# Kernel optimization log

Hardware: AMD Instinct MI355X
Metric: run time of the kernel (lower is better)

Reference implementation:

```python
import jax, jax.numpy as jnp
import numpy as np
from jax import lax

TOPK = 80
RADIUS_GAIN = 14.0
RADIUS_MIN = 1.5
RADIUS_MAX = 18.0


def _norm01(x, eps=1e-6):
    b = x.shape[0]
    flat = x.reshape(b, -1)
    mn = flat.min(axis=1).reshape(b, 1, 1, 1)
    mx = flat.max(axis=1).reshape(b, 1, 1, 1)
    return (x - mn) / (mx - mn + eps)


def _avg_pool9(x):
    # kernel 9, stride 1, pad 4, count_include_pad=True (torch default)
    s = lax.reduce_window(x, 0.0, lax.add, (1, 1, 9, 9), (1, 1, 1, 1),
                          [(0, 0), (0, 0), (4, 4), (4, 4)])
    return s / 81.0


def _max_pool5(x):
    return lax.reduce_window(x, -jnp.inf, lax.max, (1, 1, 5, 5), (1, 1, 1, 1),
                             [(0, 0), (0, 0), (2, 2), (2, 2)])


def setup_inputs() -> dict:
    key = jax.random.key(0)
    k1, k2 = jax.random.split(key)
    B, H, W = 8, 256, 256
    voxel_score_map = jax.random.uniform(k1, (B, 1, H, W), dtype=jnp.float32)
    depth = jax.random.uniform(k2, (B, 1, H, W), dtype=jnp.float32)
    return {"voxel_score_map": voxel_score_map, "depth": depth}


def reference(voxel_score_map, depth):
    dtype = voxel_score_map.dtype
    b, _, h, w = voxel_score_map.shape

    # _compact_connected_prior
    occ = (voxel_score_map > 0.2).astype(dtype)
    local_occ = _avg_pool9(occ)
    local_mass = _avg_pool9(voxel_score_map)
    compact = _norm01(local_occ * local_mass)
    score_map = voxel_score_map * compact

    # _gaussian_map: 5x5 max-pool NMS -> per-image top-k peaks
    pooled = _max_pool5(score_map)
    maxima = score_map * (score_map == pooled).astype(dtype)
    flat = maxima[:, 0].reshape(b, h * w)          # [b, h*w]
    vals, inds = lax.top_k(flat, TOPK)             # [b, k]
    vals = jnp.where(vals > 0, vals, jnp.zeros_like(vals))  # masked peaks splat 0
    ys = (inds // w).astype(dtype)
    xs = (inds % w).astype(dtype)

    z = jnp.take_along_axis(depth[:, 0].reshape(b, h * w), inds, axis=1)
    z = jnp.maximum(z, 0.001)
    radius = jnp.clip(RADIUS_GAIN / z, RADIUS_MIN, RADIUS_MAX)  # [b, k]
    sigma2 = (0.6 * radius) ** 2                                 # [b, k]

    yy = jnp.arange(h, dtype=dtype)
    xx = jnp.arange(w, dtype=dtype)
    dx = xx[None, None, None, :] - xs[:, :, None, None]   # [b, k, 1, w]
    dy = yy[None, None, :, None] - ys[:, :, None, None]   # [b, k, h, 1]
    d2 = dx ** 2 + dy ** 2                                 # [b, k, h, w]
    maps = vals[:, :, None, None] * jnp.exp(-d2 / (2.0 * sigma2[:, :, None, None] + 1e-6))
    gauss = maps.max(axis=1)[:, None]                      # [b, 1, h, w]
    return _norm01(gauss)
```

## Files before the change

### kernel.cpp

```cpp
#include <hip/hip_runtime.h>
#include <float.h>
#include <math.h>

#define BB 8
#define HH 256
#define WW 256
#define NPIX 65536
#define TOT (BB*NPIX)
#define KTOP 80
#define NTIL 64
#define TCAP 128
#define SELBINS 4096
#define SELCAP 2048
typedef unsigned long long ull;

__global__ void k_box9(const float* __restrict__ vsm, float* __restrict__ prod,
                       float* __restrict__ pmn, float* __restrict__ pmx) {
    int blk = blockIdx.x;
    int b = blk >> 6;
    int t = blk & 63;
    int ty0 = (t >> 3) << 5;
    int tx0 = (t & 7) << 5;
    int tid = threadIdx.x;

    __shared__ float val[40][40];
    __shared__ float rs_o[40][32];
    __shared__ float rs_m[40][32];

    for (int i = tid; i < 1600; i += 256) {
        int ly = i / 40, lx = i - ly * 40;
        int gy = ty0 - 4 + ly, gx = tx0 - 4 + lx;
        float v = 0.f;
        if (gy >= 0 && gy < HH && gx >= 0 && gx < WW)
            v = vsm[(b * HH + gy) * WW + gx];
        val[ly][lx] = v;
    }
    __syncthreads();

    for (int i = tid; i < 1280; i += 256) {
        int ly = i >> 5, lx = i & 31;
        float so = 0.f, sm = 0.f;
        #pragma unroll
        for (int d = 0; d < 9; ++d) {
            float v = val[ly][lx + d];
            so += (v > 0.2f) ? 1.f : 0.f;
            sm += v;
        }
        rs_o[ly][lx] = so;
        rs_m[ly][lx] = sm;
    }
    __syncthreads();

    int ox = tid & 31;
    int oy0 = (tid >> 5) << 2;
    float tmn = FLT_MAX, tmx = -FLT_MAX;
    #pragma unroll
    for (int j = 0; j < 4; ++j) {
        int oy = oy0 + j;
        float so = 0.f, sm = 0.f;
        #pragma unroll
        for (int d = 0; d < 9; ++d) {
            so += rs_o[oy + d][ox];
            sm += rs_m[oy + d][ox];
        }
        float p = (so * (1.f / 81.f)) * (sm * (1.f / 81.f));
        prod[(b * HH + ty0 + oy) * WW + tx0 + ox] = p;
        tmn = fminf(tmn, p);
        tmx = fmaxf(tmx, p);
    }

    __shared__ float smn[256], smx[256];
    smn[tid] = tmn; smx[tid] = tmx;
    __syncthreads();
    for (int off = 128; off > 0; off >>= 1) {
        if (tid < off) {
            smn[tid] = fminf(smn[tid], smn[tid + off]);
            smx[tid] = fmaxf(smx[tid], smx[tid + off]);
        }
        __syncthreads();
    }
    if (tid == 0) { pmn[blk] = smn[0]; pmx[blk] = smx[0]; }
}

__global__ void k_nms(const float* __restrict__ vsm, const float* __restrict__ prod,
                      const float* __restrict__ pmn, const float* __restrict__ pmx,
                      unsigned* __restrict__ bcnt, float* __restrict__ candV,
                      int* __restrict__ candI) {
    int blk = blockIdx.x;
    int b = blk >> 6;
    int t = blk & 63;
    int ty0 = (t >> 3) << 5;
    int tx0 = (t & 7) << 5;
    int tid = threadIdx.x;

    __shared__ float sred[2];
    if (tid < 64) {
        float mn = pmn[b * NTIL + tid];
        float mx = pmx[b * NTIL + tid];
        #pragma unroll
        for (int o = 32; o > 0; o >>= 1) {
            mn = fminf(mn, __shfl_xor(mn, o, 64));
            mx = fmaxf(mx, __shfl_xor(mx, o, 64));
        }
        if (tid == 0) { sred[0] = mn; sred[1] = mx; }
    }
    __syncthreads();
    float mnp = sred[0];
    float inv = 1.f / (sred[1] - mnp + 1e-6f);

    __shared__ float sc[36][36];
    __shared__ float hm[36][32];

    for (int i = tid; i < 1296; i += 256) {
        int ly = i / 36, lx = i - ly * 36;
        int gy = ty0 - 2 + ly, gx = tx0 - 2 + lx;
        float s = -FLT_MAX;
        if (gy >= 0 && gy < HH && gx >= 0 && gx < WW) {
            int idx = (b * HH + gy) * WW + gx;
            s = vsm[idx] * ((prod[idx] - mnp) * inv);
        }
        sc[ly][lx] = s;
    }
    __syncthreads();

    for (int i = tid; i < 1152; i += 256) {
        int ly = i >> 5, lx = i & 31;
        float m = sc[ly][lx];
        #pragma unroll
        for (int d = 1; d < 5; ++d) m = fmaxf(m, sc[ly][lx + d]);
        hm[ly][lx] = m;
    }
    __syncthreads();

    __shared__ unsigned scnt;
    __shared__ float bv[TCAP];
    __shared__ int bi[TCAP];
    if (tid == 0) scnt = 0;
    __syncthreads();

    int ox = tid & 31;
    int oy0 = (tid >> 5) << 2;
    #pragma unroll
    for (int j = 0; j < 4; ++j) {
        int oy = oy0 + j;
        float m = hm[oy][ox];
        #pragma unroll
        for (int d = 1; d < 5; ++d) m = fmaxf(m, hm[oy + d][ox]);
        float s = sc[oy + 2][ox + 2];
        if (s == m && s > 0.f) {
            unsigned p = atomicAdd(&scnt, 1u);
            if (p < TCAP) {
                bv[p] = s;
                bi[p] = (ty0 + oy) * WW + tx0 + ox;
            }
        }
    }
    __syncthreads();
    unsigned cnt = min(scnt, (unsigned)TCAP);
    if (tid == 0) bcnt[blk] = cnt;
    for (unsigned i = tid; i < cnt; i += 256) {
        candV[blk * TCAP + i] = bv[i];
        candI[blk * TCAP + i] = bi[i];
    }
}

__global__ void __launch_bounds__(1024)
k_topk(const float* __restrict__ depth, const unsigned* __restrict__ bcnt,
       const float* __restrict__ candV, const int* __restrict__ candI,
       float4* __restrict__ pk) {
    int b = blockIdx.x;
    int tid = threadIdx.x;
    __shared__ unsigned hist[SELBINS];
    __shared__ unsigned sc[1024];
    __shared__ ull keyAll[SELCAP];
    __shared__ unsigned bcs[NTIL];
    __shared__ int sBin;
    __shared__ unsigned sN;

    const float* cv = candV + b * NTIL * TCAP;
    const int* ci = candI + b * NTIL * TCAP;

    #pragma unroll
    for (int i = 0; i < SELBINS / 1024; ++i) hist[tid + i * 1024] = 0;
    if (tid < NTIL) bcs[tid] = bcnt[b * NTIL + tid];
    if (tid == 0) { sBin = 0; sN = 0; }
    __syncthreads();

    for (int i = tid; i < NTIL * TCAP; i += 1024) {
        int tile = i >> 7, o = i & (TCAP - 1);
        if ((unsigned)o < bcs[tile])
            atomicAdd(&hist[__float_as_uint(cv[i]) >> 19], 1u);
    }
    __syncthreads();

    int j0 = tid * 4;
    unsigned h0 = hist[j0], h1 = hist[j0 + 1], h2 = hist[j0 + 2], h3 = hist[j0 + 3];
    unsigned part = h0 + h1 + h2 + h3;
    sc[tid] = part;
    __syncthreads();
    for (int off = 1; off < 1024; off <<= 1) {
        unsigned v = (tid + off < 1024) ? sc[tid + off] : 0u;
        __syncthreads();
        sc[tid] += v;
        __syncthreads();
    }
    unsigned excl = sc[tid] - part;
    unsigned suf3 = excl + h3;
    unsigned suf2 = suf3 + h2;
    unsigned suf1 = suf2 + h1;
    unsigned suf0 = suf1 + h0;
    if (suf0 >= KTOP && suf0 - h0 < KTOP) sBin = j0;
    if (suf1 >= KTOP && suf1 - h1 < KTOP) sBin = j0 + 1;
    if (suf2 >= KTOP && suf2 - h2 < KTOP) sBin = j0 + 2;
    if (suf3 >= KTOP && suf3 - h3 < KTOP) sBin = j0 + 3;
    __syncthreads();

    int B = sBin;
    for (int i = tid; i < NTIL * TCAP; i += 1024) {
        int tile = i >> 7, o = i & (TCAP - 1);
        if ((unsigned)o < bcs[tile]) {
            unsigned bits = __float_as_uint(cv[i]);
            if ((int)(bits >> 19) >= B) {
                unsigned p = atomicAdd(&sN, 1u);
                if (p < SELCAP)
                    keyAll[p] = ((ull)bits << 32) | (ull)(0xFFFFFFFFu - (unsigned)ci[i]);
            }
        }
    }
    __syncthreads();
    unsigned n = min(sN, (unsigned)SELCAP);
    unsigned P = 128; while (P < n) P <<= 1;
    for (unsigned i = n + tid; i < P; i += 1024) keyAll[i] = 0ull;
    __syncthreads();

    for (unsigned k = 2; k <= P; k <<= 1) {
        for (unsigned j = k >> 1; j > 0; j >>= 1) {
            for (unsigned i = tid; i < P; i += 1024) {
                unsigned ixj = i ^ j;
                if (ixj > i) {
                    ull a = keyAll[i], c = keyAll[ixj];
                    bool up = ((i & k) == 0);
                    if (up ? (a > c) : (a < c)) { keyAll[i] = c; keyAll[ixj] = a; }
                }
            }
            __syncthreads();
        }
    }

    if (tid < KTOP) {
        unsigned K = min((unsigned)KTOP, n);
        float plog = -INFINITY, fx = 0.f, fy = 0.f, c = 0.f;
        if ((unsigned)tid < K) {
            ull key = keyAll[P - 1 - tid];
            unsigned bits = (unsigned)(key >> 32);
            int idx = (int)(0xFFFFFFFFu - (unsigned)(key & 0xFFFFFFFFu));
            float val = __uint_as_float(bits);
            plog = log2f(val);
            fx = (float)(idx & 255);
            fy = (float)(idx >> 8);
            float z = fmaxf(depth[b * NPIX + idx], 0.001f);
            float r = fminf(fmaxf(14.f / z, 1.5f), 18.f);
            float s2 = 0.36f * r * r;
            c = 1.44269504f / (2.f * s2 + 1e-6f);
        }
        pk[b * KTOP + tid] = make_float4(plog, fx, fy, c);
    }
}

__global__ void k_splat(const float4* __restrict__ pk, float* __restrict__ gauss,
                        float* __restrict__ gmn, float* __restrict__ gmx) {
    int blk = blockIdx.x;
    int b = blk >> 6;
    int y0 = (blk & 63) << 2;
    int x = threadIdx.x;

    __shared__ float4 lp[KTOP];
    if (x < KTOP) lp[x] = pk[b * KTOP + x];
    __syncthreads();

    float fx = (float)x;
    float fy = (float)y0;
    float g0 = -INFINITY, g1 = -INFINITY, g2 = -INFINITY, g3 = -INFINITY;
    #pragma unroll 4
    for (int k = 0; k < KTOP; ++k) {
        float4 q = lp[k];
        float dx = fx - q.y;
        float dx2 = dx * dx;
        float dy = fy - q.z;
        float d2;
        d2 = fmaf(dy, dy, dx2);           g0 = fmaxf(g0, fmaf(-d2, q.w, q.x));
        float dyb = dy + 1.f;
        d2 = fmaf(dyb, dyb, dx2);         g1 = fmaxf(g1, fmaf(-d2, q.w, q.x));
        float dyc = dy + 2.f;
        d2 = fmaf(dyc, dyc, dx2);         g2 = fmaxf(g2, fmaf(-d2, q.w, q.x));
        float dyd = dy + 3.f;
        d2 = fmaf(dyd, dyd, dx2);         g3 = fmaxf(g3, fmaf(-d2, q.w, q.x));
    }
    float v0 = exp2f(g0), v1 = exp2f(g1), v2 = exp2f(g2), v3 = exp2f(g3);
    int base = (b * HH + y0) * WW + x;
    gauss[base]          = v0;
    gauss[base + WW]     = v1;
    gauss[base + 2 * WW] = v2;
    gauss[base + 3 * WW] = v3;

    float tmn = fminf(fminf(v0, v1), fminf(v2, v3));
    float tmx = fmaxf(fmaxf(v0, v1), fmaxf(v2, v3));
    __shared__ float smn[256], smx[256];
    smn[x] = tmn; smx[x] = tmx;
    __syncthreads();
    for (int off = 128; off > 0; off >>= 1) {
        if (x < off) {
            smn[x] = fminf(smn[x], smn[x + off]);
            smx[x] = fmaxf(smx[x], smx[x + off]);
        }
        __syncthreads();
    }
    if (x == 0) { gmn[blk] = smn[0]; gmx[blk] = smx[0]; }
}

__global__ void k_norm(const float* __restrict__ gauss, const float* __restrict__ gmn,
                       const float* __restrict__ gmx, float* __restrict__ out) {
    int blk = blockIdx.x;
    int b = blk >> 6;
    int tid = threadIdx.x;

    __shared__ float sred[2];
    if (tid < 64) {
        float mn = gmn[b * NTIL + tid];
        float mx = gmx[b * NTIL + tid];
        #pragma unroll
        for (int o = 32; o > 0; o >>= 1) {
            mn = fminf(mn, __shfl_xor(mn, o, 64));
            mx = fmaxf(mx, __shfl_xor(mx, o, 64));
        }
        if (tid == 0) { sred[0] = mn; sred[1] = mx; }
    }
    __syncthreads();
    float mn = sred[0];
    float inv = 1.f / (sred[1] - mn + 1e-6f);

    int i = blk * 256 + tid;
    float4 v = ((const float4*)gauss)[i];
    v.x = (v.x - mn) * inv;
    v.y = (v.y - mn) * inv;
    v.z = (v.z - mn) * inv;
    v.w = (v.w - mn) * inv;
    ((float4*)out)[i] = v;
}

extern "C" void kernel_launch(void* const* d_in, const int* in_sizes, int n_in,
                              void* d_out, int out_size, void* d_ws, size_t ws_size,
                              hipStream_t stream) {
    const float* vsm   = (const float*)d_in[0];
    const float* depth = (const float*)d_in[1];
    float* out = (float*)d_out;

    float4* pk = (float4*)d_ws;
    float* prod = (float*)(pk + BB * KTOP);
    float* gauss = prod + TOT;
    float* pmn = gauss + TOT;
    float* pmx = pmn + BB * NTIL;
    float* gmn = pmx + BB * NTIL;
    float* gmx = gmn + BB * NTIL;
    unsigned* bcnt = (unsigned*)(gmx + BB * NTIL);
    float* candV = (float*)(bcnt + BB * NTIL);
    int* candI = (int*)(candV + BB * NTIL * TCAP);

    const int NBLK = BB * NTIL;

    k_box9 <<<NBLK, 256, 0, stream>>>(vsm, prod, pmn, pmx);
    k_nms  <<<NBLK, 256, 0, stream>>>(vsm, prod, pmn, pmx, bcnt, candV, candI);
    k_topk <<<BB, 1024, 0, stream>>>(depth, bcnt, candV, candI, pk);
    k_splat<<<NBLK, 256, 0, stream>>>(pk, gauss, gmn, gmx);
    k_norm <<<NBLK, 256, 0, stream>>>(gauss, gmn, gmx, out);
}
```

Measured before the change: 42.45 us.

## Fuse per-image top-k selection into splat kernel, recomputed per block

Removes the separate 8-block top-k kernel and the pk workspace round trip. Each splat block now redundantly computes its image's top-k via histogram, compaction and bitonic sort with 256 threads before splatting its rows. This aims to eliminate a launch and a low-parallelism serial stage, at the cost of 64x redundant selection work, extra L2 traffic and larger shared memory per block.

```diff
diff --git a/kernel.cpp b/kernel.cpp
--- a/kernel.cpp
+++ b/kernel.cpp
@@ -12,71 +12,51 @@
 #define TCAP 128
 #define SELBINS 4096
 #define SELCAP 2048
+#define NBLK (BB*NTIL)
 typedef unsigned long long ull;
 
 __global__ void k_box9(const float* __restrict__ vsm, float* __restrict__ prod,
                        float* __restrict__ pmn, float* __restrict__ pmx) {
     int blk = blockIdx.x;
-    int b = blk >> 6;
-    int t = blk & 63;
-    int ty0 = (t >> 3) << 5;
-    int tx0 = (t & 7) << 5;
+    int b = blk >> 6, t = blk & 63;
+    int ty0 = (t >> 3) << 5, tx0 = (t & 7) << 5;
     int tid = threadIdx.x;
-
     __shared__ float val[40][40];
     __shared__ float rs_o[40][32];
     __shared__ float rs_m[40][32];
-
     for (int i = tid; i < 1600; i += 256) {
         int ly = i / 40, lx = i - ly * 40;
         int gy = ty0 - 4 + ly, gx = tx0 - 4 + lx;
         float v = 0.f;
-        if (gy >= 0 && gy < HH && gx >= 0 && gx < WW)
-            v = vsm[(b * HH + gy) * WW + gx];
+        if (gy >= 0 && gy < HH && gx >= 0 && gx < WW) v = vsm[(b * HH + gy) * WW + gx];
         val[ly][lx] = v;
     }
     __syncthreads();
-
     for (int i = tid; i < 1280; i += 256) {
         int ly = i >> 5, lx = i & 31;
         float so = 0.f, sm = 0.f;
         #pragma unroll
-        for (int d = 0; d < 9; ++d) {
-            float v = val[ly][lx + d];
-            so += (v > 0.2f) ? 1.f : 0.f;
-            sm += v;
-        }
-        rs_o[ly][lx] = so;
-        rs_m[ly][lx] = sm;
-    }
-    __syncthreads();
-
-    int ox = tid & 31;
-    int oy0 = (tid >> 5) << 2;
+        for (int d = 0; d < 9; ++d) { float v = val[ly][lx + d]; so += (v > 0.2f) ? 1.f : 0.f; sm += v; }
+        rs_o[ly][lx] = so; rs_m[ly][lx] = sm;
+    }
+    __syncthreads();
+    int ox = tid & 31, oy0 = (tid >> 5) << 2;
     float tmn = FLT_MAX, tmx = -FLT_MAX;
     #pragma unroll
     for (int j = 0; j < 4; ++j) {
         int oy = oy0 + j;
         float so = 0.f, sm = 0.f;
         #pragma unroll
-        for (int d = 0; d < 9; ++d) {
-            so += rs_o[oy + d][ox];
-            sm += rs_m[oy + d][ox];
-        }
+        for (int d = 0; d < 9; ++d) { so += rs_o[oy + d][ox]; sm += rs_m[oy + d][ox]; }
         float p = (so * (1.f / 81.f)) * (sm * (1.f / 81.f));
         prod[(b * HH + ty0 + oy) * WW + tx0 + ox] = p;
-        tmn = fminf(tmn, p);
-        tmx = fmaxf(tmx, p);
-    }
-
+        tmn = fminf(tmn, p); tmx = fmaxf(tmx, p);
+    }
     __shared__ float smn[256], smx[256];
     smn[tid] = tmn; smx[tid] = tmx;
     __syncthreads();
     for (int off = 128; off > 0; off >>= 1) {
-        if (tid < off) {
-            smn[tid] = fminf(smn[tid], smn[tid + off]);
-            smx[tid] = fmaxf(smx[tid], smx[tid + off]);
-        }
+        if (tid < off) { smn[tid] = fminf(smn[tid], smn[tid + off]); smx[tid] = fmaxf(smx[tid], smx[tid + off]); }
         __syncthreads();
     }
     if (tid == 0) { pmn[blk] = smn[0]; pmx[blk] = smx[0]; }
@@ -87,30 +67,22 @@
                       unsigned* __restrict__ bcnt, float* __restrict__ candV,
                       int* __restrict__ candI) {
     int blk = blockIdx.x;
-    int b = blk >> 6;
-    int t = blk & 63;
-    int ty0 = (t >> 3) << 5;
-    int tx0 = (t & 7) << 5;
+    int b = blk >> 6, t = blk & 63;
+    int ty0 = (t >> 3) << 5, tx0 = (t & 7) << 5;
     int tid = threadIdx.x;
-
     __shared__ float sred[2];
     if (tid < 64) {
         float mn = pmn[b * NTIL + tid];
         float mx = pmx[b * NTIL + tid];
         #pragma unroll
-        for (int o = 32; o > 0; o >>= 1) {
-            mn = fminf(mn, __shfl_xor(mn, o, 64));
-            mx = fmaxf(mx, __shfl_xor(mx, o, 64));
-        }
+        for (int o = 32; o > 0; o >>= 1) { mn = fminf(mn, __shfl_xor(mn, o, 64)); mx = fmaxf(mx, __shfl_xor(mx, o, 64)); }
         if (tid == 0) { sred[0] = mn; sred[1] = mx; }
     }
     __syncthreads();
     float mnp = sred[0];
     float inv = 1.f / (sred[1] - mnp + 1e-6f);
-
     __shared__ float sc[36][36];
     __shared__ float hm[36][32];
-
     for (int i = tid; i < 1296; i += 256) {
         int ly = i / 36, lx = i - ly * 36;
         int gy = ty0 - 2 + ly, gx = tx0 - 2 + lx;
@@ -122,7 +94,6 @@
         sc[ly][lx] = s;
     }
     __syncthreads();
-
     for (int i = tid; i < 1152; i += 256) {
         int ly = i >> 5, lx = i & 31;
         float m = sc[ly][lx];
@@ -131,15 +102,12 @@
         hm[ly][lx] = m;
     }
     __syncthreads();
-
     __shared__ unsigned scnt;
     __shared__ float bv[TCAP];
     __shared__ int bi[TCAP];
     if (tid == 0) scnt = 0;
     __syncthreads();
-
-    int ox = tid & 31;
-    int oy0 = (tid >> 5) << 2;
+    int ox = tid & 31, oy0 = (tid >> 5) << 2;
     #pragma unroll
     for (int j = 0; j < 4; ++j) {
         int oy = oy0 + j;
@@ -149,10 +117,7 @@
         float s = sc[oy + 2][ox + 2];
         if (s == m && s > 0.f) {
             unsigned p = atomicAdd(&scnt, 1u);
-            if (p < TCAP) {
-                bv[p] = s;
-                bi[p] = (ty0 + oy) * WW + tx0 + ox;
-            }
+            if (p < TCAP) { bv[p] = s; bi[p] = (ty0 + oy) * WW + tx0 + ox; }
         }
     }
     __syncthreads();
@@ -164,158 +129,153 @@
     }
 }
 
-__global__ void __launch_bounds__(1024)
-k_topk(const float* __restrict__ depth, const unsigned* __restrict__ bcnt,
-       const float* __restrict__ candV, const int* __restrict__ candI,
-       float4* __restrict__ pk) {
-    int b = blockIdx.x;
+__global__ void __launch_bounds__(256)
+k_splatk(const float* __restrict__ depth, const unsigned* __restrict__ bcnt,
+         const float* __restrict__ candV, const int* __restrict__ candI,
+         float* __restrict__ gauss, float* __restrict__ gmn, float* __restrict__ gmx) {
+    int blk = blockIdx.x;
+    int b = blk >> 6;
     int tid = threadIdx.x;
-    __shared__ unsigned hist[SELBINS];
-    __shared__ unsigned sc[1024];
-    __shared__ ull keyAll[SELCAP];
-    __shared__ unsigned bcs[NTIL];
+
+    __shared__ struct {
+        unsigned hist[SELBINS];
+        ull keyAll[SELCAP];
+        unsigned bcs[NTIL];
+        unsigned scan[256];
+    } tk;
+    __shared__ float4 lp[KTOP];
+    __shared__ float r0[256], r1[256];
     __shared__ int sBin;
     __shared__ unsigned sN;
 
-    const float* cv = candV + b * NTIL * TCAP;
-    const int* ci = candI + b * NTIL * TCAP;
-
-    #pragma unroll
-    for (int i = 0; i < SELBINS / 1024; ++i) hist[tid + i * 1024] = 0;
-    if (tid < NTIL) bcs[tid] = bcnt[b * NTIL + tid];
-    if (tid == 0) { sBin = 0; sN = 0; }
-    __syncthreads();
-
-    for (int i = tid; i < NTIL * TCAP; i += 1024) {
-        int tile = i >> 7, o = i & (TCAP - 1);
-        if ((unsigned)o < bcs[tile])
-            atomicAdd(&hist[__float_as_uint(cv[i]) >> 19], 1u);
-    }
-    __syncthreads();
-
-    int j0 = tid * 4;
-    unsigned h0 = hist[j0], h1 = hist[j0 + 1], h2 = hist[j0 + 2], h3 = hist[j0 + 3];
-    unsigned part = h0 + h1 + h2 + h3;
-    sc[tid] = part;
-    __syncthreads();
-    for (int off = 1; off < 1024; off <<= 1) {
-        unsigned v = (tid + off < 1024) ? sc[tid + off] : 0u;
-        __syncthreads();
-        sc[tid] += v;
-        __syncthreads();
-    }
-    unsigned excl = sc[tid] - part;
-    unsigned suf3 = excl + h3;
-    unsigned suf2 = suf3 + h2;
-    unsigned suf1 = suf2 + h1;
-    unsigned suf0 = suf1 + h0;
-    if (suf0 >= KTOP && suf0 - h0 < KTOP) sBin = j0;
-    if (suf1 >= KTOP && suf1 - h1 < KTOP) sBin = j0 + 1;
-    if (suf2 >= KTOP && suf2 - h2 < KTOP) sBin = j0 + 2;
-    if (suf3 >= KTOP && suf3 - h3 < KTOP) sBin = j0 + 3;
-    __syncthreads();
-
-    int B = sBin;
-    for (int i = tid; i < NTIL * TCAP; i += 1024) {
-        int tile = i >> 7, o = i & (TCAP - 1);
-        if ((unsigned)o < bcs[tile]) {
-            unsigned bits = __float_as_uint(cv[i]);
-            if ((int)(bits >> 19) >= B) {
-                unsigned p = atomicAdd(&sN, 1u);
-                if (p < SELCAP)
-                    keyAll[p] = ((ull)bits << 32) | (ull)(0xFFFFFFFFu - (unsigned)ci[i]);
-            }
-        }
-    }
-    __syncthreads();
-    unsigned n = min(sN, (unsigned)SELCAP);
-    unsigned P = 128; while (P < n) P <<= 1;
-    for (unsigned i = n + tid; i < P; i += 1024) keyAll[i] = 0ull;
-    __syncthreads();
-
-    for (unsigned k = 2; k <= P; k <<= 1) {
-        for (unsigned j = k >> 1; j > 0; j >>= 1) {
-            for (unsigned i = tid; i < P; i += 1024) {
-                unsigned ixj = i ^ j;
-                if (ixj > i) {
-                    ull a = keyAll[i], c = keyAll[ixj];
-                    bool up = ((i & k) == 0);
-                    if (up ? (a > c) : (a < c)) { keyAll[i] = c; keyAll[ixj] = a; }
+    {
+        const float* cv = candV + b * NTIL * TCAP;
+        const int*   ci = candI + b * NTIL * TCAP;
+        for (int i = tid; i < SELBINS; i += 256) tk.hist[i] = 0;
+        if (tid < NTIL) tk.bcs[tid] = bcnt[b * NTIL + tid];
+        if (tid == 0) { sBin = 0; sN = 0; }
+        __syncthreads();
+
+        for (int i = tid; i < NTIL * TCAP; i += 256) {
+            int tile = i >> 7, o = i & (TCAP - 1);
+            if ((unsigned)o < tk.bcs[tile])
+                atomicAdd(&tk.hist[__float_as_uint(cv[i]) >> 19], 1u);
+        }
+        __syncthreads();
+
+        int j0 = tid * 16;
+        unsigned part = 0;
+        #pragma unroll
+        for (int j = 0; j < 16; ++j) part += tk.hist[j0 + j];
+        tk.scan[tid] = part;
+        __syncthreads();
+        for (int off = 1; off < 256; off <<= 1) {
+            unsigned v = (tid + off < 256) ? tk.scan[tid + off] : 0u;
+            __syncthreads();
+            tk.scan[tid] += v;
+            __syncthreads();
+        }
+        unsigned run = tk.scan[tid] - part;
+        for (int j = 15; j >= 0; --j) {
+            unsigned h = tk.hist[j0 + j];
+            run += h;
+            if (run >= KTOP && run - h < KTOP) sBin = j0 + j;
+        }
+        __syncthreads();
+
+        int B = sBin;
+        for (int i = tid; i < NTIL * TCAP; i += 256) {
+            int tile = i >> 7, o = i & (TCAP - 1);
+            if ((unsigned)o < tk.bcs[tile]) {
+                unsigned bits = __float_as_uint(cv[i]);
+                if ((int)(bits >> 19) >= B) {
+                    unsigned p = atomicAdd(&sN, 1u);
+                    if (p < SELCAP)
+                        tk.keyAll[p] = ((ull)bits << 32) | (ull)(0xFFFFFFFFu - (unsigned)ci[i]);
                 }
             }
+        }
+        __syncthreads();
+        unsigned n = min(sN, (unsigned)SELCAP);
+        unsigned P = 128; while (P < n) P <<= 1;
+        for (unsigned i = n + tid; i < P; i += 256) tk.keyAll[i] = 0ull;
+        __syncthreads();
+
+        for (unsigned k = 2; k <= P; k <<= 1) {
+            for (unsigned j = k >> 1; j > 0; j >>= 1) {
+                for (unsigned i = tid; i < P; i += 256) {
+                    unsigned ixj = i ^ j;
+                    if (ixj > i) {
+                        ull a = tk.keyAll[i], c = tk.keyAll[ixj];
+                        bool up = ((i & k) == 0);
+                        if (up ? (a > c) : (a < c)) { tk.keyAll[i] = c; tk.keyAll[ixj] = a; }
+                    }
+                }
+                __syncthreads();
+            }
+        }
+
+        if (tid < KTOP) {
+            unsigned K = min((unsigned)KTOP, n);
+            float plog = -INFINITY, fx = 0.f, fy = 0.f, c = 0.f;
+            if ((unsigned)tid < K) {
+                ull key = tk.keyAll[P - 1 - tid];
+                unsigned bits = (unsigned)(key >> 32);
+                int idx = (int)(0xFFFFFFFFu - (unsigned)(key & 0xFFFFFFFFu));
+                float val = __uint_as_float(bits);
+                plog = log2f(val);
+                fx = (float)(idx & 255);
+                fy = (float)(idx >> 8);
+                float z = fmaxf(depth[b * NPIX + idx], 0.001f);
+                float r = fminf(fmaxf(14.f / z, 1.5f), 18.f);
+                float s2 = 0.36f * r * r;
+                c = 1.44269504f / (2.f * s2 + 1e-6f);
+            }
+            lp[tid] = make_float4(plog, fx, fy, c);
+        }
+        __syncthreads();
+    }
+
+    {
+        int y0 = (blk & 63) << 2;
+        float fx = (float)tid;
+        float fy = (float)y0;
+        float g0 = -INFINITY, g1 = -INFINITY, g2 = -INFINITY, g3 = -INFINITY;
+        #pragma unroll 4
+        for (int k = 0; k < KTOP; ++k) {
+            float4 q = lp[k];
+            float dx = fx - q.y;
+            float dx2 = dx * dx;
+            float dy = fy - q.z;
+            float d2;
+            d2 = fmaf(dy, dy, dx2);          g0 = fmaxf(g0, fmaf(-d2, q.w, q.x));
+            float dyb = dy + 1.f;
+            d2 = fmaf(dyb, dyb, dx2);        g1 = fmaxf(g1, fmaf(-d2, q.w, q.x));
+            float dyc = dy + 2.f;
+            d2 = fmaf(dyc, dyc, dx2);        g2 = fmaxf(g2, fmaf(-d2, q.w, q.x));
+            float dyd = dy + 3.f;
+            d2 = fmaf(dyd, dyd, dx2);        g3 = fmaxf(g3, fmaf(-d2, q.w, q.x));
+        }
+        float v0 = exp2f(g0), v1 = exp2f(g1), v2 = exp2f(g2), v3 = exp2f(g3);
+        int base = (b * HH + y0) * WW + tid;
+        gauss[base]          = v0;
+        gauss[base + WW]     = v1;
+        gauss[base + 2 * WW] = v2;
+        gauss[base + 3 * WW] = v3;
+
+        float tmn = fminf(fminf(v0, v1), fminf(v2, v3));
+        float tmx = fmaxf(fmaxf(v0, v1), fmaxf(v2, v3));
+        r0[tid] = tmn; r1[tid] = tmx;
+        __syncthreads();
+        for (int off = 128; off > 0; off >>= 1) {
+            if (tid < off) {
+                r0[tid] = fminf(r0[tid], r0[tid + off]);
+                r1[tid] = fmaxf(r1[tid], r1[tid + off]);
+            }
             __syncthreads();
         }
-    }
-
-    if (tid < KTOP) {
-        unsigned K = min((unsigned)KTOP, n);
-        float plog = -INFINITY, fx = 0.f, fy = 0.f, c = 0.f;
-        if ((unsigned)tid < K) {
-            ull key = keyAll[P - 1 - tid];
-            unsigned bits = (unsigned)(key >> 32);
-            int idx = (int)(0xFFFFFFFFu - (unsigned)(key & 0xFFFFFFFFu));
-            float val = __uint_as_float(bits);
-            plog = log2f(val);
-            fx = (float)(idx & 255);
-            fy = (float)(idx >> 8);
-            float z = fmaxf(depth[b * NPIX + idx], 0.001f);
-            float r = fminf(fmaxf(14.f / z, 1.5f), 18.f);
-            float s2 = 0.36f * r * r;
-            c = 1.44269504f / (2.f * s2 + 1e-6f);
-        }
-        pk[b * KTOP + tid] = make_float4(plog, fx, fy, c);
-    }
-}
-
-__global__ void k_splat(const float4* __restrict__ pk, float* __restrict__ gauss,
-                        float* __restrict__ gmn, float* __restrict__ gmx) {
-    int blk = blockIdx.x;
-    int b = blk >> 6;
-    int y0 = (blk & 63) << 2;
-    int x = threadIdx.x;
-
-    __shared__ float4 lp[KTOP];
-    if (x < KTOP) lp[x] = pk[b * KTOP + x];
-    __syncthreads();
-
-    float fx = (float)x;
-    float fy = (float)y0;
-    float g0 = -INFINITY, g1 = -INFINITY, g2 = -INFINITY, g3 = -INFINITY;
-    #pragma unroll 4
-    for (int k = 0; k < KTOP; ++k) {
-        float4 q = lp[k];
-        float dx = fx - q.y;
-        float dx2 = dx * dx;
-        float dy = fy - q.z;
-        float d2;
-        d2 = fmaf(dy, dy, dx2);           g0 = fmaxf(g0, fmaf(-d2, q.w, q.x));
-        float dyb = dy + 1.f;
-        d2 = fmaf(dyb, dyb, dx2);         g1 = fmaxf(g1, fmaf(-d2, q.w, q.x));
-        float dyc = dy + 2.f;
-        d2 = fmaf(dyc, dyc, dx2);         g2 = fmaxf(g2, fmaf(-d2, q.w, q.x));
-        float dyd = dy + 3.f;
-        d2 = fmaf(dyd, dyd, dx2);         g3 = fmaxf(g3, fmaf(-d2, q.w, q.x));
-    }
-    float v0 = exp2f(g0), v1 = exp2f(g1), v2 = exp2f(g2), v3 = exp2f(g3);
-    int base = (b * HH + y0) * WW + x;
-    gauss[base]          = v0;
-    gauss[base + WW]     = v1;
-    gauss[base + 2 * WW] = v2;
-    gauss[base + 3 * WW] = v3;
-
-    float tmn = fminf(fminf(v0, v1), fminf(v2, v3));
-    float tmx = fmaxf(fmaxf(v0, v1), fmaxf(v2, v3));
-    __shared__ float smn[256], smx[256];
-    smn[x] = tmn; smx[x] = tmx;
-    __syncthreads();
-    for (int off = 128; off > 0; off >>= 1) {
-        if (x < off) {
-            smn[x] = fminf(smn[x], smn[x + off]);
-            smx[x] = fmaxf(smx[x], smx[x + off]);
-        }
-        __syncthreads();
-    }
-    if (x == 0) { gmn[blk] = smn[0]; gmx[blk] = smx[0]; }
+        if (tid == 0) { gmn[blk] = r0[0]; gmx[blk] = r1[0]; }
+    }
 }
 
 __global__ void k_norm(const float* __restrict__ gauss, const float* __restrict__ gmn,
@@ -323,22 +283,17 @@
     int blk = blockIdx.x;
     int b = blk >> 6;
     int tid = threadIdx.x;
-
     __shared__ float sred[2];
     if (tid < 64) {
         float mn = gmn[b * NTIL + tid];
         float mx = gmx[b * NTIL + tid];
         #pragma unroll
-        for (int o = 32; o > 0; o >>= 1) {
-            mn = fminf(mn, __shfl_xor(mn, o, 64));
-            mx = fmaxf(mx, __shfl_xor(mx, o, 64));
-        }
+        for (int o = 32; o > 0; o >>= 1) { mn = fminf(mn, __shfl_xor(mn, o, 64)); mx = fmaxf(mx, __shfl_xor(mx, o, 64)); }
         if (tid == 0) { sred[0] = mn; sred[1] = mx; }
     }
     __syncthreads();
     float mn = sred[0];
     float inv = 1.f / (sred[1] - mn + 1e-6f);
-
     int i = blk * 256 + tid;
     float4 v = ((const float4*)gauss)[i];
     v.x = (v.x - mn) * inv;
@@ -355,22 +310,18 @@
     const float* depth = (const float*)d_in[1];
     float* out = (float*)d_out;
 
-    float4* pk = (float4*)d_ws;
-    float* prod = (float*)(pk + BB * KTOP);
+    float* prod  = (float*)d_ws;
     float* gauss = prod + TOT;
-    float* pmn = gauss + TOT;
-    float* pmx = pmn + BB * NTIL;
-    float* gmn = pmx + BB * NTIL;
-    float* gmx = gmn + BB * NTIL;
-    unsigned* bcnt = (unsigned*)(gmx + BB * NTIL);
-    float* candV = (float*)(bcnt + BB * NTIL);
-    int* candI = (int*)(candV + BB * NTIL * TCAP);
-
-    const int NBLK = BB * NTIL;
-
-    k_box9 <<<NBLK, 256, 0, stream>>>(vsm, prod, pmn, pmx);
-    k_nms  <<<NBLK, 256, 0, stream>>>(vsm, prod, pmn, pmx, bcnt, candV, candI);
-    k_topk <<<BB, 1024, 0, stream>>>(depth, bcnt, candV, candI, pk);
-    k_splat<<<NBLK, 256, 0, stream>>>(pk, gauss, gmn, gmx);
-    k_norm <<<NBLK, 256, 0, stream>>>(gauss, gmn, gmx, out);
-}
+    float* pmn   = gauss + TOT;
+    float* pmx   = pmn + NBLK;
+    float* gmn   = pmx + NBLK;
+    float* gmx   = gmn + NBLK;
+    unsigned* bcnt = (unsigned*)(gmx + NBLK);
+    float* candV = (float*)(bcnt + NBLK);
+    int*   candI = (int*)(candV + NBLK * TCAP);
+
+    k_box9  <<<NBLK, 256, 0, stream>>>(vsm, prod, pmn, pmx);
+    k_nms   <<<NBLK, 256, 0, stream>>>(vsm, prod, pmn, pmx, bcnt, candV, candI);
+    k_splatk<<<NBLK, 256, 0, stream>>>(depth, bcnt, candV, candI, gauss, gmn, gmx);
+    k_norm  <<<NBLK, 256, 0, stream>>>(gauss, gmn, gmx, out);
+}
```

Result: slower. 57.67 us (+35.9%).
